# Performance work log

Measured on AMD Instinct MI355X. Metric: run time of the kernel, lower is better.

## Reference

```python
import jax, jax.numpy as jnp
import numpy as np

N_NODES = 50000


def gcn_conv(x, W, b, src, dst, n_nodes):
    # PyG GCNConv: h = D^{-1/2} (A + I) D^{-1/2} (x W) + b
    h = x @ W  # [N, out]
    # degree with self loops: deg[i] = in_degree(i) + 1
    deg = jax.ops.segment_sum(jnp.ones_like(dst, dtype=h.dtype), dst, num_segments=n_nodes) + 1.0
    dis = jax.lax.rsqrt(deg)  # deg >= 1 always
    norm = dis[src] * dis[dst]  # [E]
    # gather-scale-scatter over edges
    agg = jax.ops.segment_sum(h[src] * norm[:, None], dst, num_segments=n_nodes)
    # self-loop contribution: norm_ii = dis[i]^2
    agg = agg + h * (dis * dis)[:, None]
    return agg + b


def setup_inputs() -> dict:
    key = jax.random.key(0)
    k1, k2, k3, k4, k5, k6 = jax.random.split(key, 6)
    latent, hidden, out = 64, 96, 64
    x = jax.random.normal(k1, (N_NODES, latent), dtype=jnp.float32)
    edge_index = jax.random.randint(k2, (2, 800000), 0, N_NODES, dtype=jnp.int64)
    W1 = jax.random.normal(k3, (latent, hidden), dtype=jnp.float32) / np.sqrt(latent)
    b1 = jnp.zeros((hidden,), dtype=jnp.float32)
    W2 = jax.random.normal(k4, (hidden, out), dtype=jnp.float32) / np.sqrt(hidden)
    b2 = jnp.zeros((out,), dtype=jnp.float32)
    return {"x": x, "edge_index": edge_index, "W1": W1, "b1": b1, "W2": W2, "b2": b2}


def reference(x, edge_index, W1, b1, W2, b2):
    src, dst = edge_index[0], edge_index[1]
    n = x.shape[0]
    h = jax.nn.relu(gcn_conv(x, W1, b1, src, dst, n))
    out = jax.nn.sigmoid(gcn_conv(h, W2, b2, src, dst, n))
    return out
```

## Files before the change

### kernel.cpp

```cpp
#include <hip/hip_runtime.h>
#include <hip/hip_bf16.h>
#include <hip/hip_fp16.h>

typedef float nt_f4 __attribute__((ext_vector_type(4)));

constexpr int G1 = 96;
constexpr int RNODES = 25088;
constexpr int CAP = 64;

__global__ __launch_bounds__(256) void histo_kernel(const int* __restrict__ dst,
                                                    unsigned short* __restrict__ hist,
                                                    int E, int chunk, int npad2) {
    __shared__ unsigned int h32[RNODES / 2];
    int g = blockIdx.x;
    int base = blockIdx.y * RNODES;
    int e0 = g * chunk;
    int e1 = min(e0 + chunk, E);
    for (int i = threadIdx.x; i < RNODES / 2; i += 256) h32[i] = 0;
    __syncthreads();
    for (int e = e0 + threadIdx.x; e < e1; e += 256) {
        int d = dst[e] - base;
        if ((unsigned)d < (unsigned)RNODES) atomicAdd(&h32[d >> 1], 1u << ((d & 1) * 16));
    }
    __syncthreads();
    for (int i = threadIdx.x; i < RNODES; i += 256)
        hist[(size_t)g * npad2 + base + i] =
            (unsigned short)((h32[i >> 1] >> ((i & 1) * 16)) & 0xFFFFu);
}

__global__ __launch_bounds__(256) void colscan_cast_kernel(
    const unsigned short* __restrict__ hist, unsigned short* __restrict__ off16,
    int* __restrict__ cnt, float* __restrict__ dis, const float* __restrict__ x,
    __half* __restrict__ Th, int N, int npad2) {
    __shared__ float sdis[256];
    int n0 = blockIdx.x * 256;
    int d = n0 + threadIdx.x;
    float dv = 0.f;
    if (d < N) {
        unsigned int hv[G1];
#pragma unroll
        for (int g = 0; g < G1; ++g) hv[g] = hist[(size_t)g * npad2 + d];
        int run = 0;
#pragma unroll
        for (int g = 0; g < G1; ++g) {
            off16[(size_t)g * npad2 + d] = (unsigned short)run;
            run += (int)hv[g];
        }
        cnt[d] = run;
        dv = rsqrtf((float)run + 1.0f);
        dis[d] = dv;
    }
    sdis[threadIdx.x] = dv;
    __syncthreads();
    int total = min(256, N - n0) * 64;
    size_t base_elem = (size_t)n0 * 64;
    for (int l = threadIdx.x * 8; l < total; l += 256 * 8) {
        float dn = sdis[l >> 6];
        float4 a = *(const float4*)(x + base_elem + l);
        float4 b = *(const float4*)(x + base_elem + l + 4);
        __half2 h[4];
        h[0] = __floats2half2_rn(a.x * dn, a.y * dn);
        h[1] = __floats2half2_rn(a.z * dn, a.w * dn);
        h[2] = __floats2half2_rn(b.x * dn, b.y * dn);
        h[3] = __floats2half2_rn(b.z * dn, b.w * dn);
        *(float4*)(Th + base_elem + l) = *(float4*)h;
    }
}

__global__ __launch_bounds__(256) void fill_bucket16_kernel(
    const int* __restrict__ src, const int* __restrict__ dst,
    const unsigned short* __restrict__ off16, unsigned short* __restrict__ csr16,
    int E, int chunk, int npad2) {
    __shared__ unsigned int c16[RNODES / 2];
    int g = blockIdx.x;
    int base = blockIdx.y * RNODES;
    const unsigned int* op = (const unsigned int*)(off16 + (size_t)g * npad2 + base);
    for (int i = threadIdx.x; i < RNODES / 2; i += 256) c16[i] = op[i];
    __syncthreads();
    int e0 = g * chunk;
    int e1 = min(e0 + chunk, E);
    for (int e = e0 + threadIdx.x; e < e1; e += 256) {
        int d = dst[e] - base;
        if ((unsigned)d < (unsigned)RNODES) {
            unsigned int sh = (d & 1) * 16;
            unsigned int old = atomicAdd(&c16[d >> 1], 1u << sh);
            unsigned int rank = (old >> sh) & 0xFFFFu;
            if (rank < CAP) csr16[(size_t)(base + d) * CAP + rank] = (unsigned short)src[e];
        }
    }
}

__global__ void zero_int_kernel(int* __restrict__ p, int N) {
    int i = blockIdx.x * blockDim.x + threadIdx.x;
    if (i < N) p[i] = 0;
}
__global__ void degree_int_kernel(const int* __restrict__ dst, int* __restrict__ cnt, int E) {
    int i = blockIdx.x * blockDim.x + threadIdx.x;
    if (i < E) atomicAdd(&cnt[dst[i]], 1);
}
__global__ void dis_from_cnt_kernel(const int* __restrict__ cnt, float* __restrict__ dis, int N) {
    int i = blockIdx.x * blockDim.x + threadIdx.x;
    if (i < N) dis[i] = rsqrtf((float)cnt[i] + 1.0f);
}
__global__ __launch_bounds__(1024) void scan_kernel(const int* __restrict__ cnt,
                                                    int* __restrict__ cursor, int N) {
    constexpr int T = 1024;
    __shared__ int sums[T];
    int t = threadIdx.x;
    int ch = (N + T - 1) / T;
    int base = t * ch;
    int local = 0;
    for (int k = 0; k < ch; ++k) {
        int idx = base + k;
        if (idx < N) local += cnt[idx];
    }
    sums[t] = local;
    __syncthreads();
    for (int off = 1; off < T; off <<= 1) {
        int add = (t >= off) ? sums[t - off] : 0;
        __syncthreads();
        sums[t] += add;
        __syncthreads();
    }
    int run = sums[t] - local;
    for (int k = 0; k < ch; ++k) {
        int idx = base + k;
        if (idx < N) {
            cursor[idx] = run;
            run += cnt[idx];
        }
    }
}
__global__ void fill_atomic_kernel(const int* __restrict__ src, const int* __restrict__ dst,
                                   int* __restrict__ cursor_mut, int* __restrict__ csr_src,
                                   int E) {
    int e = blockIdx.x * blockDim.x + threadIdx.x;
    if (e >= E) return;
    int pos = atomicAdd(&cursor_mut[dst[e]], 1);
    csr_src[pos] = src[e];
}
__global__ void cast_scale_kernel(const float* __restrict__ X, const float* __restrict__ dis,
                                  __half* __restrict__ Th, int N) {
    int i = blockIdx.x * blockDim.x + threadIdx.x;
    int n = i >> 3;
    if (n >= N) return;
    int c = (i & 7) * 8;
    float dn = dis[n];
    float4 a = *(const float4*)(X + (size_t)n * 64 + c);
    float4 b = *(const float4*)(X + (size_t)n * 64 + c + 4);
    __half2 h[4];
    h[0] = __floats2half2_rn(a.x * dn, a.y * dn);
    h[1] = __floats2half2_rn(a.z * dn, a.w * dn);
    h[2] = __floats2half2_rn(b.x * dn, b.y * dn);
    h[3] = __floats2half2_rn(b.z * dn, b.w * dn);
    *(float4*)(Th + (size_t)n * 64 + c) = *(float4*)h;
}

__device__ __forceinline__ void gather_batch16(const unsigned short* __restrict__ bucket,
                                               int j0, int scnt,
                                               const __half* __restrict__ Xh, int c,
                                               float a[16]) {
    uint4 raw = *(const uint4*)(bucket + j0);
    unsigned int w[4] = {raw.x, raw.y, raw.z, raw.w};
    float4 r0[8], r1[8];
#pragma unroll
    for (int k = 0; k < 8; ++k) {
        if (k < scnt) {
            int s = (w[k >> 1] >> ((k & 1) * 16)) & 0xFFFF;
            const __half* row = Xh + (size_t)s * 64 + c;
            r0[k] = *(const float4*)(row);
            r1[k] = *(const float4*)(row + 8);
        }
    }
#pragma unroll
    for (int k = 0; k < 8; ++k) {
        if (k < scnt) {
            const __half2* h0 = (const __half2*)&r0[k];
            const __half2* h1 = (const __half2*)&r1[k];
#pragma unroll
            for (int q = 0; q < 4; ++q) {
                float2 f0 = __half22float2(h0[q]);
                float2 f1 = __half22float2(h1[q]);
                a[2 * q] += f0.x;
                a[2 * q + 1] += f0.y;
                a[8 + 2 * q] += f1.x;
                a[8 + 2 * q + 1] += f1.y;
            }
        }
    }
}

__device__ __forceinline__ void gather_batch32(const unsigned short* __restrict__ bucket,
                                               int j0, int scnt,
                                               const __half* __restrict__ Xh, int c,
                                               float a[16]) {
    uint4 rawA = *(const uint4*)(bucket + j0);
    uint4 rawB = *(const uint4*)(bucket + j0 + 8);
    unsigned int w[8] = {rawA.x, rawA.y, rawA.z, rawA.w, rawB.x, rawB.y, rawB.z, rawB.w};
    float4 r0[16], r1[16];
#pragma unroll
    for (int k = 0; k < 16; ++k) {
        if (k < scnt) {
            int s = (w[k >> 1] >> ((k & 1) * 16)) & 0xFFFF;
            const __half* row = Xh + (size_t)s * 64 + c;
            r0[k] = *(const float4*)(row);
            r1[k] = *(const float4*)(row + 8);
        }
    }
#pragma unroll
    for (int k = 0; k < 16; ++k) {
        if (k < scnt) {
            const __half2* h0 = (const __half2*)&r0[k];
            const __half2* h1 = (const __half2*)&r1[k];
#pragma unroll
            for (int q = 0; q < 4; ++q) {
                float2 f0 = __half22float2(h0[q]);
                float2 f1 = __half22float2(h1[q]);
                a[2 * q] += f0.x;
                a[2 * q + 1] += f0.y;
                a[8 + 2 * q] += f1.x;
                a[8 + 2 * q + 1] += f1.y;
            }
        }
    }
}

__device__ __forceinline__ void add_row16(const __half* __restrict__ row, float a[16]) {
    float4 r0 = *(const float4*)(row);
    float4 r1 = *(const float4*)(row + 8);
    const __half2* h0 = (const __half2*)&r0;
    const __half2* h1 = (const __half2*)&r1;
#pragma unroll
    for (int q = 0; q < 4; ++q) {
        float2 f0 = __half22float2(h0[q]);
        float2 f1 = __half22float2(h1[q]);
        a[2 * q] += f0.x;
        a[2 * q + 1] += f0.y;
        a[8 + 2 * q] += f1.x;
        a[8 + 2 * q + 1] += f1.y;
    }
}

template <int CAPT, typename IDX>
__global__ __launch_bounds__(256) void agg0_kernel(const int* __restrict__ cursor,
                                                   const int* __restrict__ cnt,
                                                   const IDX* __restrict__ csr,
                                                   const float* __restrict__ dis,
                                                   const __half* __restrict__ Xh,
                                                   __half* __restrict__ Yh, int N) {
    int i = blockIdx.x * 256 + threadIdx.x;
    int n = i >> 2;
    if (n >= N) return;
    int c = (i & 3) * 16;
    float a[16] = {};
    int cn = cnt[n];
    if (CAPT) {
        cn = min(cn, CAPT);
        const unsigned short* bucket = (const unsigned short*)csr + (size_t)n * CAPT;
        for (int j0 = 0; j0 < cn; j0 += 8) {
            int m = cn - j0;
            gather_batch16(bucket, j0, m < 8 ? m : 8, Xh, c, a);
        }
    } else {
        int beg = cursor[n];
        for (int j = beg; j < beg + cn; ++j)
            add_row16(Xh + (size_t)((int)csr[j]) * 64 + c, a);
    }
    add_row16(Xh + (size_t)n * 64 + c, a);
    float dn = dis[n];
    __half2 o[8];
#pragma unroll
    for (int q = 0; q < 8; ++q)
        o[q] = __floats2half2_rn(a[2 * q] * dn, a[2 * q + 1] * dn);
    __half* yp = Yh + (size_t)n * 64 + c;
    *(float4*)(yp) = ((float4*)o)[0];
    *(float4*)(yp + 8) = ((float4*)o)[1];
}

template <int CAPT, typename IDX>
__global__ __launch_bounds__(256) void agg0_gemm_kernel(
    const int* __restrict__ cursor, const int* __restrict__ cnt,
    const IDX* __restrict__ csr, const float* __restrict__ dis,
    const __half* __restrict__ Xh, const float* __restrict__ W1,
    const float* __restrict__ b1, const float* __restrict__ W2,
    __half* __restrict__ Th2, int N) {
    constexpr int XS = 100;
    __shared__ float Xs[64 * XS];
    __shared__ float Ws[6144];
    const int t = threadIdx.x;
    const int n0 = blockIdx.x * 64;
    const int tn = t >> 4;
    const int tf = t & 15;

    for (int i = t; i < 6144 / 4; i += 256)
        ((float4*)Ws)[i] = ((const float4*)W1)[i];

    {
        int n = n0 + (t >> 2);
        int c = (t & 3) * 16;
        float a[16] = {};
        float dn = 0.f;
        if (n < N) {
            int cn = cnt[n];
            if (CAPT) {
                cn = min(cn, CAPT);
                const unsigned short* bucket = (const unsigned short*)csr + (size_t)n * CAPT;
                for (int j0 = 0; j0 < cn; j0 += 16) {
                    int m = cn - j0;
                    gather_batch32(bucket, j0, m < 16 ? m : 16, Xh, c, a);
                }
            } else {
                int beg = cursor[n];
                for (int j = beg; j < beg + cn; ++j)
                    add_row16(Xh + (size_t)((int)csr[j]) * 64 + c, a);
            }
            add_row16(Xh + (size_t)n * 64 + c, a);
            dn = dis[n];
        }
        float* xp = Xs + (size_t)(t >> 2) * XS + c;
#pragma unroll
        for (int q = 0; q < 4; ++q) {
            float4 v = make_float4(a[4 * q] * dn, a[4 * q + 1] * dn, a[4 * q + 2] * dn,
                                   a[4 * q + 3] * dn);
            *(float4*)(xp + 4 * q) = v;
        }
    }
    float breg[6];
#pragma unroll
    for (int j = 0; j < 6; ++j) breg[j] = b1[tf * 6 + j];
    __syncthreads();

    float h[4][6] = {};
    for (int k0 = 0; k0 < 64; k0 += 4) {
        float4 xv[4];
#pragma unroll
        for (int i = 0; i < 4; ++i) xv[i] = *(const float4*)(Xs + (tn * 4 + i) * XS + k0);
        float wv[4][6];
#pragma unroll
        for (int j4 = 0; j4 < 4; ++j4)
#pragma unroll
            for (int j = 0; j < 3; ++j) {
                float2 w2 = *(const float2*)(Ws + (k0 + j4) * 96 + tf * 6 + 2 * j);
                wv[j4][2 * j] = w2.x;
                wv[j4][2 * j + 1] = w2.y;
            }
#pragma unroll
        for (int i = 0; i < 4; ++i) {
            const float xk[4] = {xv[i].x, xv[i].y, xv[i].z, xv[i].w};
#pragma unroll
            for (int j4 = 0; j4 < 4; ++j4)
#pragma unroll
                for (int j = 0; j < 6; ++j) h[i][j] += xk[j4] * wv[j4][j];
        }
    }
#pragma unroll
    for (int i = 0; i < 4; ++i)
#pragma unroll
        for (int j = 0; j < 6; ++j) h[i][j] = fmaxf(h[i][j] + breg[j], 0.f);
    __syncthreads();

#pragma unroll
    for (int i = 0; i < 4; ++i)
#pragma unroll
        for (int j = 0; j < 6; ++j) Xs[(tn * 4 + i) * XS + tf * 6 + j] = h[i][j];
    for (int i = t; i < 6144 / 4; i += 256)
        ((float4*)Ws)[i] = ((const float4*)W2)[i];
    __syncthreads();

    float acc[4][4] = {};
    for (int k0 = 0; k0 < 96; k0 += 4) {
        float4 xv[4];
#pragma unroll
        for (int i = 0; i < 4; ++i) xv[i] = *(const float4*)(Xs + (tn * 4 + i) * XS + k0);
        float wv[4][4];
#pragma unroll
        for (int j4 = 0; j4 < 4; ++j4)
#pragma unroll
            for (int j = 0; j < 2; ++j) {
                float2 w2 = *(const float2*)(Ws + (k0 + j4) * 64 + tf * 4 + 2 * j);
                wv[j4][2 * j] = w2.x;
                wv[j4][2 * j + 1] = w2.y;
            }
#pragma unroll
        for (int i = 0; i < 4; ++i) {
            const float xk[4] = {xv[i].x, xv[i].y, xv[i].z, xv[i].w};
#pragma unroll
            for (int j4 = 0; j4 < 4; ++j4)
#pragma unroll
                for (int j = 0; j < 4; ++j) acc[i][j] += xk[j4] * wv[j4][j];
        }
    }
#pragma unroll
    for (int i = 0; i < 4; ++i) {
        int n = n0 + tn * 4 + i;
        if (n < N) {
            float dn = dis[n];
            __half* op = Th2 + (size_t)n * 64 + tf * 4;
            *(__half2*)(op) = __floats2half2_rn(acc[i][0] * dn, acc[i][1] * dn);
            *(__half2*)(op + 2) = __floats2half2_rn(acc[i][2] * dn, acc[i][3] * dn);
        }
    }
}

__global__ __launch_bounds__(256) void gemm12_kernel(const __half* __restrict__ Yh,
                                                     const float* __restrict__ W1,
                                                     const float* __restrict__ b1,
                                                     const float* __restrict__ W2,
                                                     const float* __restrict__ dis,
                                                     __half* __restrict__ Th2, int N) {
    constexpr int XS = 100;
    __shared__ float Xs[64 * XS];
    __shared__ float Ws[6144];
    const int n0 = blockIdx.x * 64;
    const int t = threadIdx.x;
    const int tn = t >> 4;
    const int tf = t & 15;

    for (int i = t; i < 6144 / 4; i += 256)
        ((float4*)Ws)[i] = ((const float4*)W1)[i];
    for (int i = t; i < 512; i += 256) {
        int row = i >> 3;
        int c8 = (i & 7) * 8;
        float4 raw = make_float4(0.f, 0.f, 0.f, 0.f);
        if (n0 + row < N) raw = *(const float4*)(Yh + (size_t)(n0 + row) * 64 + c8);
        const __half2* hp = (const __half2*)&raw;
        float* p = Xs + row * XS + c8;
#pragma unroll
        for (int q = 0; q < 4; ++q) {
            float2 f = __half22float2(hp[q]);
            p[2 * q] = f.x;
            p[2 * q + 1] = f.y;
        }
    }
    float breg[6];
#pragma unroll
    for (int j = 0; j < 6; ++j) breg[j] = b1[tf * 6 + j];
    __syncthreads();

    float h[4][6] = {};
    for (int k0 = 0; k0 < 64; k0 += 4) {
        float4 xv[4];
#pragma unroll
        for (int i = 0; i < 4; ++i) xv[i] = *(const float4*)(Xs + (tn * 4 + i) * XS + k0);
        float wv[4][6];
#pragma unroll
        for (int j4 = 0; j4 < 4; ++j4)
#pragma unroll
            for (int j = 0; j < 3; ++j) {
                float2 w2 = *(const float2*)(Ws + (k0 + j4) * 96 + tf * 6 + 2 * j);
                wv[j4][2 * j] = w2.x;
                wv[j4][2 * j + 1] = w2.y;
            }
#pragma unroll
        for (int i = 0; i < 4; ++i) {
            const float xk[4] = {xv[i].x, xv[i].y, xv[i].z, xv[i].w};
#pragma unroll
            for (int j4 = 0; j4 < 4; ++j4)
#pragma unroll
                for (int j = 0; j < 6; ++j) h[i][j] += xk[j4] * wv[j4][j];
        }
    }
#pragma unroll
    for (int i = 0; i < 4; ++i)
#pragma unroll
        for (int j = 0; j < 6; ++j) h[i][j] = fmaxf(h[i][j] + breg[j], 0.f);
    __syncthreads();

#pragma unroll
    for (int i = 0; i < 4; ++i)
#pragma unroll
        for (int j = 0; j < 6; ++j) Xs[(tn * 4 + i) * XS + tf * 6 + j] = h[i][j];
    for (int i = t; i < 6144 / 4; i += 256)
        ((float4*)Ws)[i] = ((const float4*)W2)[i];
    __syncthreads();

    float acc[4][4] = {};
    for (int k0 = 0; k0 < 96; k0 += 4) {
        float4 xv[4];
#pragma unroll
        for (int i = 0; i < 4; ++i) xv[i] = *(const float4*)(Xs + (tn * 4 + i) * XS + k0);
        float wv[4][4];
#pragma unroll
        for (int j4 = 0; j4 < 4; ++j4)
#pragma unroll
            for (int j = 0; j < 2; ++j) {
                float2 w2 = *(const float2*)(Ws + (k0 + j4) * 64 + tf * 4 + 2 * j);
                wv[j4][2 * j] = w2.x;
                wv[j4][2 * j + 1] = w2.y;
            }
#pragma unroll
        for (int i = 0; i < 4; ++i) {
            const float xk[4] = {xv[i].x, xv[i].y, xv[i].z, xv[i].w};
#pragma unroll
            for (int j4 = 0; j4 < 4; ++j4)
#pragma unroll
                for (int j = 0; j < 4; ++j) acc[i][j] += xk[j4] * wv[j4][j];
        }
    }
#pragma unroll
    for (int i = 0; i < 4; ++i) {
        int n = n0 + tn * 4 + i;
        if (n < N) {
            float dn = dis[n];
            __half* op = Th2 + (size_t)n * 64 + tf * 4;
            *(__half2*)(op) = __floats2half2_rn(acc[i][0] * dn, acc[i][1] * dn);
            *(__half2*)(op + 2) = __floats2half2_rn(acc[i][2] * dn, acc[i][3] * dn);
        }
    }
}

template <int CAPT, typename IDX>
__global__ __launch_bounds__(256) void agg1_kernel(const int* __restrict__ cursor,
                                                   const int* __restrict__ cnt,
                                                   const IDX* __restrict__ csr,
                                                   const float* __restrict__ dis,
                                                   const __half* __restrict__ Xh,
                                                   const float* __restrict__ b,
                                                   float* __restrict__ out, int N) {
    int i = blockIdx.x * 256 + threadIdx.x;
    int n = i >> 2;
    if (n >= N) return;
    int c = (i & 3) * 16;
    float a[16] = {};
    int cn = cnt[n];
    if (CAPT) {
        cn = min(cn, CAPT);
        const unsigned short* bucket = (const unsigned short*)csr + (size_t)n * CAPT;
        for (int j0 = 0; j0 < cn; j0 += 16) {
            int m = cn - j0;
            gather_batch32(bucket, j0, m < 16 ? m : 16, Xh, c, a);
        }
    } else {
        int beg = cursor[n];
        for (int j = beg; j < beg + cn; ++j)
            add_row16(Xh + (size_t)((int)csr[j]) * 64 + c, a);
    }
    add_row16(Xh + (size_t)n * 64 + c, a);
    float dn = dis[n];
    float r[16];
#pragma unroll
    for (int q = 0; q < 16; ++q) r[q] = 1.f / (1.f + expf(-(a[q] * dn + b[c + q])));
    float* op = out + (size_t)n * 64 + c;
    __builtin_nontemporal_store((nt_f4){r[0], r[1], r[2], r[3]}, (nt_f4*)(op));
    __builtin_nontemporal_store((nt_f4){r[4], r[5], r[6], r[7]}, (nt_f4*)(op + 4));
    __builtin_nontemporal_store((nt_f4){r[8], r[9], r[10], r[11]}, (nt_f4*)(op + 8));
    __builtin_nontemporal_store((nt_f4){r[12], r[13], r[14], r[15]}, (nt_f4*)(op + 12));
}

extern "C" void kernel_launch(void* const* d_in, const int* in_sizes, int n_in,
                              void* d_out, int out_size, void* d_ws, size_t ws_size,
                              hipStream_t stream) {
    const float* x  = (const float*)d_in[0];
    const int*   ei = (const int*)d_in[1];
    const float* W1 = (const float*)d_in[2];
    const float* b1 = (const float*)d_in[3];
    const float* W2 = (const float*)d_in[4];
    const float* b2 = (const float*)d_in[5];

    constexpr int LAT = 64;
    const int E = in_sizes[1] / 2;
    const int N = in_sizes[0] / LAT;
    const int* src = ei;
    const int* dst = ei + E;

    const int B = 256;
    auto blocks = [](long total, int b) { return (int)((total + b - 1) / b); };

    const int ranges = (N + RNODES - 1) / RNODES;
    const int npad2 = ranges * RNODES;
    const int chunk = (E + G1 - 1) / G1;

    long nmax = (npad2 > N) ? npad2 : N;
    size_t Na = (size_t)((nmax + 1023) / 1024) * 1024;
    size_t Epad = (size_t)((E + 3) / 4) * 4;
    size_t csrBytes = (size_t)Na * CAP * 2;
    if (csrBytes < Epad * 4) csrBytes = Epad * 4;
    csrBytes = (csrBytes + 15) / 16 * 16;

    int* cnt      = (int*)d_ws;
    int* cursor   = cnt + Na;
    int* cursmut  = cursor + Na;
    float* dis    = (float*)(cursmut + Na);
    char* csr_raw = (char*)(dis + Na);
    unsigned short* csr16 = (unsigned short*)csr_raw;
    int*            csr32 = (int*)csr_raw;
    unsigned short* hist  = (unsigned short*)(csr_raw + csrBytes);
    unsigned short* off16 = hist + (size_t)G1 * npad2;
    __half* Th  = (__half*)(off16 + (size_t)G1 * npad2);
    __half* Th2 = Th + Na * 64;
    __half* Yh  = Th2 + Na * 64;

    size_t need = (char*)(Yh + Na * 64) - (char*)d_ws;
    bool fast = (ws_size >= need) && (chunk < 65536) && (ranges <= 16) && (N <= 65535);

    if (fast) {
        dim3 g2(G1, ranges);
        histo_kernel<<<g2, 256, 0, stream>>>(dst, hist, E, chunk, npad2);
        colscan_cast_kernel<<<blocks(N, 256), 256, 0, stream>>>(hist, off16, cnt, dis, x, Th,
                                                                N, npad2);
        fill_bucket16_kernel<<<g2, 256, 0, stream>>>(src, dst, off16, csr16, E, chunk, npad2);
        agg0_gemm_kernel<CAP, unsigned short>
            <<<blocks(N, 64), 256, 0, stream>>>(nullptr, cnt, csr16, dis, Th, W1, b1, W2,
                                                Th2, N);
        agg1_kernel<CAP, unsigned short>
            <<<blocks((long)N * 4, B), B, 0, stream>>>(nullptr, cnt, csr16, dis, Th2, b2,
                                                       (float*)d_out, N);
    } else {
        zero_int_kernel<<<blocks(N, B), B, 0, stream>>>(cnt, N);
        degree_int_kernel<<<blocks(E, B), B, 0, stream>>>(dst, cnt, E);
        dis_from_cnt_kernel<<<blocks(N, B), B, 0, stream>>>(cnt, dis, N);
        scan_kernel<<<1, 1024, 0, stream>>>(cnt, cursor, N);
        hipMemcpyAsync(cursmut, cursor, (size_t)N * sizeof(int), hipMemcpyDeviceToDevice, stream);
        fill_atomic_kernel<<<blocks(E, B), B, 0, stream>>>(src, dst, cursmut, csr32, E);
        cast_scale_kernel<<<blocks((long)N * 8, B), B, 0, stream>>>(x, dis, Th, N);
        agg0_kernel<0, int>
            <<<blocks((long)N * 4, B), B, 0, stream>>>(cursor, cnt, csr32, dis, Th, Yh, N);
        gemm12_kernel<<<blocks(N, 64), 256, 0, stream>>>(Yh, W1, b1, W2, dis, Th2, N);
        agg1_kernel<0, int>
            <<<blocks((long)N * 4, B), B, 0, stream>>>(cursor, cnt, csr32, dis, Th2, b2,
                                                       (float*)d_out, N);
    }
}
```

Baseline: 184.4 us.

## Replace histogram/scan bucket build with single-pass global-atomic bucket fill

Removes the three-kernel LDS histogram, column scan and per-chunk bucket fill used to build the fixed-capacity CSR. Each edge now takes its slot directly with one global atomicAdd on the destination's counter, and degree normalisation moves into a separate cast kernel that reads the final counts. This cuts two passes over dst and the large hist/off16 scratch arrays. The cost is heavy global atomic traffic and a nondeterministic neighbour order within each bucket.

Result: no change. 181.7 us (-1.5%).

```diff
diff --git a/kernel.cpp b/kernel.cpp
--- a/kernel.cpp
+++ b/kernel.cpp
@@ -4,96 +4,43 @@
 
 typedef float nt_f4 __attribute__((ext_vector_type(4)));
 
-constexpr int G1 = 96;
-constexpr int RNODES = 25088;
 constexpr int CAP = 64;
-
-__global__ __launch_bounds__(256) void histo_kernel(const int* __restrict__ dst,
-                                                    unsigned short* __restrict__ hist,
-                                                    int E, int chunk, int npad2) {
-    __shared__ unsigned int h32[RNODES / 2];
-    int g = blockIdx.x;
-    int base = blockIdx.y * RNODES;
-    int e0 = g * chunk;
-    int e1 = min(e0 + chunk, E);
-    for (int i = threadIdx.x; i < RNODES / 2; i += 256) h32[i] = 0;
-    __syncthreads();
-    for (int e = e0 + threadIdx.x; e < e1; e += 256) {
-        int d = dst[e] - base;
-        if ((unsigned)d < (unsigned)RNODES) atomicAdd(&h32[d >> 1], 1u << ((d & 1) * 16));
-    }
-    __syncthreads();
-    for (int i = threadIdx.x; i < RNODES; i += 256)
-        hist[(size_t)g * npad2 + base + i] =
-            (unsigned short)((h32[i >> 1] >> ((i & 1) * 16)) & 0xFFFFu);
-}
-
-__global__ __launch_bounds__(256) void colscan_cast_kernel(
-    const unsigned short* __restrict__ hist, unsigned short* __restrict__ off16,
-    int* __restrict__ cnt, float* __restrict__ dis, const float* __restrict__ x,
-    __half* __restrict__ Th, int N, int npad2) {
-    __shared__ float sdis[256];
-    int n0 = blockIdx.x * 256;
-    int d = n0 + threadIdx.x;
-    float dv = 0.f;
-    if (d < N) {
-        unsigned int hv[G1];
-#pragma unroll
-        for (int g = 0; g < G1; ++g) hv[g] = hist[(size_t)g * npad2 + d];
-        int run = 0;
-#pragma unroll
-        for (int g = 0; g < G1; ++g) {
-            off16[(size_t)g * npad2 + d] = (unsigned short)run;
-            run += (int)hv[g];
-        }
-        cnt[d] = run;
-        dv = rsqrtf((float)run + 1.0f);
-        dis[d] = dv;
-    }
-    sdis[threadIdx.x] = dv;
-    __syncthreads();
-    int total = min(256, N - n0) * 64;
-    size_t base_elem = (size_t)n0 * 64;
-    for (int l = threadIdx.x * 8; l < total; l += 256 * 8) {
-        float dn = sdis[l >> 6];
-        float4 a = *(const float4*)(x + base_elem + l);
-        float4 b = *(const float4*)(x + base_elem + l + 4);
-        __half2 h[4];
-        h[0] = __floats2half2_rn(a.x * dn, a.y * dn);
-        h[1] = __floats2half2_rn(a.z * dn, a.w * dn);
-        h[2] = __floats2half2_rn(b.x * dn, b.y * dn);
-        h[3] = __floats2half2_rn(b.z * dn, b.w * dn);
-        *(float4*)(Th + base_elem + l) = *(float4*)h;
-    }
-}
-
-__global__ __launch_bounds__(256) void fill_bucket16_kernel(
-    const int* __restrict__ src, const int* __restrict__ dst,
-    const unsigned short* __restrict__ off16, unsigned short* __restrict__ csr16,
-    int E, int chunk, int npad2) {
-    __shared__ unsigned int c16[RNODES / 2];
-    int g = blockIdx.x;
-    int base = blockIdx.y * RNODES;
-    const unsigned int* op = (const unsigned int*)(off16 + (size_t)g * npad2 + base);
-    for (int i = threadIdx.x; i < RNODES / 2; i += 256) c16[i] = op[i];
-    __syncthreads();
-    int e0 = g * chunk;
-    int e1 = min(e0 + chunk, E);
-    for (int e = e0 + threadIdx.x; e < e1; e += 256) {
-        int d = dst[e] - base;
-        if ((unsigned)d < (unsigned)RNODES) {
-            unsigned int sh = (d & 1) * 16;
-            unsigned int old = atomicAdd(&c16[d >> 1], 1u << sh);
-            unsigned int rank = (old >> sh) & 0xFFFFu;
-            if (rank < CAP) csr16[(size_t)(base + d) * CAP + rank] = (unsigned short)src[e];
-        }
-    }
-}
 
 __global__ void zero_int_kernel(int* __restrict__ p, int N) {
     int i = blockIdx.x * blockDim.x + threadIdx.x;
     if (i < N) p[i] = 0;
 }
+
+__global__ __launch_bounds__(256) void fill_bucket_atomic16_kernel(
+    const int* __restrict__ src, const int* __restrict__ dst,
+    int* __restrict__ cnt, unsigned short* __restrict__ csr16, int E) {
+    int e = blockIdx.x * 256 + threadIdx.x;
+    if (e >= E) return;
+    int d = dst[e];
+    int s = src[e];
+    int rank = atomicAdd(&cnt[d], 1);
+    if (rank < CAP) csr16[(size_t)d * CAP + rank] = (unsigned short)s;
+}
+
+__global__ __launch_bounds__(256) void cast_scale_dis_kernel(
+    const float* __restrict__ X, const int* __restrict__ cnt,
+    float* __restrict__ dis, __half* __restrict__ Th, int N) {
+    int i = blockIdx.x * blockDim.x + threadIdx.x;
+    int n = i >> 3;
+    if (n >= N) return;
+    int c = (i & 7) * 8;
+    float dn = rsqrtf((float)cnt[n] + 1.0f);
+    if ((i & 7) == 0) dis[n] = dn;
+    float4 a = *(const float4*)(X + (size_t)n * 64 + c);
+    float4 b = *(const float4*)(X + (size_t)n * 64 + c + 4);
+    __half2 h[4];
+    h[0] = __floats2half2_rn(a.x * dn, a.y * dn);
+    h[1] = __floats2half2_rn(a.z * dn, a.w * dn);
+    h[2] = __floats2half2_rn(b.x * dn, b.y * dn);
+    h[3] = __floats2half2_rn(b.z * dn, b.w * dn);
+    *(float4*)(Th + (size_t)n * 64 + c) = *(float4*)h;
+}
+
 __global__ void degree_int_kernel(const int* __restrict__ dst, int* __restrict__ cnt, int E) {
     int i = blockIdx.x * blockDim.x + threadIdx.x;
     if (i < E) atomicAdd(&cnt[dst[i]], 1);
@@ -566,12 +513,7 @@
     const int B = 256;
     auto blocks = [](long total, int b) { return (int)((total + b - 1) / b); };
 
-    const int ranges = (N + RNODES - 1) / RNODES;
-    const int npad2 = ranges * RNODES;
-    const int chunk = (E + G1 - 1) / G1;
-
-    long nmax = (npad2 > N) ? npad2 : N;
-    size_t Na = (size_t)((nmax + 1023) / 1024) * 1024;
+    size_t Na = (size_t)((N + 1023) / 1024) * 1024;
     size_t Epad = (size_t)((E + 3) / 4) * 4;
     size_t csrBytes = (size_t)Na * CAP * 2;
     if (csrBytes < Epad * 4) csrBytes = Epad * 4;
@@ -584,21 +526,17 @@
     char* csr_raw = (char*)(dis + Na);
     unsigned short* csr16 = (unsigned short*)csr_raw;
     int*            csr32 = (int*)csr_raw;
-    unsigned short* hist  = (unsigned short*)(csr_raw + csrBytes);
-    unsigned short* off16 = hist + (size_t)G1 * npad2;
-    __half* Th  = (__half*)(off16 + (size_t)G1 * npad2);
+    __half* Th  = (__half*)(csr_raw + csrBytes);
     __half* Th2 = Th + Na * 64;
     __half* Yh  = Th2 + Na * 64;
 
     size_t need = (char*)(Yh + Na * 64) - (char*)d_ws;
-    bool fast = (ws_size >= need) && (chunk < 65536) && (ranges <= 16) && (N <= 65535);
+    bool fast = (ws_size >= need) && (N <= 65535);
 
     if (fast) {
-        dim3 g2(G1, ranges);
-        histo_kernel<<<g2, 256, 0, stream>>>(dst, hist, E, chunk, npad2);
-        colscan_cast_kernel<<<blocks(N, 256), 256, 0, stream>>>(hist, off16, cnt, dis, x, Th,
-                                                                N, npad2);
-        fill_bucket16_kernel<<<g2, 256, 0, stream>>>(src, dst, off16, csr16, E, chunk, npad2);
+        zero_int_kernel<<<blocks(N, B), B, 0, stream>>>(cnt, N);
+        fill_bucket_atomic16_kernel<<<blocks(E, B), B, 0, stream>>>(src, dst, cnt, csr16, E);
+        cast_scale_dis_kernel<<<blocks((long)N * 8, B), B, 0, stream>>>(x, cnt, dis, Th, N);
         agg0_gemm_kernel<CAP, unsigned short>
             <<<blocks(N, 64), 256, 0, stream>>>(nullptr, cnt, csr16, dis, Th, W1, b1, W2,
                                                 Th2, N);
```
